# Performance work log

Measured on AMD Instinct MI355X. Metric: run time of the kernel, lower is better.

## Reference

```python
import jax, jax.numpy as jnp
import numpy as np

D = 1024      # embedding_size
H = 16        # num_heads
HD = D // H   # head_size
EPS = 1e-5


def setup_inputs() -> dict:
    key = jax.random.key(0)
    ks = jax.random.split(key, 12)
    s_in = 1.0 / np.sqrt(D)
    s_hid = 1.0 / np.sqrt(4 * D)
    return {
        "x": jax.random.normal(ks[0], (2, 2048, D), dtype=jnp.float32),
        # per-head projections, no bias: [H, D, HD]
        "Wq": jax.random.normal(ks[1], (H, D, HD), dtype=jnp.float32) * s_in,
        "Wk": jax.random.normal(ks[2], (H, D, HD), dtype=jnp.float32) * s_in,
        "Wv": jax.random.normal(ks[3], (H, D, HD), dtype=jnp.float32) * s_in,
        "Wo": jax.random.normal(ks[4], (D, D), dtype=jnp.float32) * s_in,
        "bo": jnp.zeros((D,), dtype=jnp.float32),
        "W1": jax.random.normal(ks[5], (D, 4 * D), dtype=jnp.float32) * s_in,
        "b1": jnp.zeros((4 * D,), dtype=jnp.float32),
        "W2": jax.random.normal(ks[6], (4 * D, D), dtype=jnp.float32) * s_hid,
        "b2": jnp.zeros((D,), dtype=jnp.float32),
        "g1": jnp.ones((D,), dtype=jnp.float32),
        "be1": jnp.zeros((D,), dtype=jnp.float32),
        "g2": jnp.ones((D,), dtype=jnp.float32),
        "be2": jnp.zeros((D,), dtype=jnp.float32),
    }


def _layernorm(x, g, b):
    mu = jnp.mean(x, axis=-1, keepdims=True)
    var = jnp.mean(jnp.square(x - mu), axis=-1, keepdims=True)
    return (x - mu) * jax.lax.rsqrt(var + EPS) * g + b


def _block(x, Wq, Wk, Wv, Wo, bo, W1, b1, W2, b2, g1, be1, g2, be2):
    B, T, _ = x.shape
    h = _layernorm(x, g1, be1)
    # per-head projections: [B, H, T, HD]
    q = jnp.einsum('btd,hde->bhte', h, Wq)
    k = jnp.einsum('btd,hde->bhte', h, Wk)
    v = jnp.einsum('btd,hde->bhte', h, Wv)
    # NOTE: original scales by embedding_size**-0.5 (x.shape[-1]), not head_size
    scores = jnp.einsum('bhte,bhse->bhts', q, k) * (D ** -0.5)
    mask = jnp.tril(jnp.ones((T, T), dtype=bool))
    scores = jnp.where(mask, scores, -jnp.inf)
    attn = jax.nn.softmax(scores, axis=-1)           # dropout = identity (eval)
    out = jnp.einsum('bhts,bhse->bhte', attn, v)      # [B, H, T, HD]
    out = out.transpose(0, 2, 1, 3).reshape(B, T, D)  # concat heads
    x = x + (out @ Wo + bo)
    h2 = _layernorm(x, g2, be2)
    ffn = jax.nn.relu(h2 @ W1 + b1) @ W2 + b2
    return x + ffn


def reference(x, Wq, Wk, Wv, Wo, bo, W1, b1, W2, b2, g1, be1, g2, be2):
    return _block(x, Wq, Wk, Wv, Wo, bo, W1, b1, W2, b2, g1, be1, g2, be2)
```

## Files before the change

kernel.cpp:

```cpp
#include <hip/hip_runtime.h>
#include <stdint.h>

typedef unsigned short u16;
typedef __attribute__((ext_vector_type(8))) __bf16 bf16x8;
typedef __attribute__((ext_vector_type(4))) float f32x4;

#define D_EMB 1024
#define NHEAD 16
#define HDIM 64
#define TSEQ 2048
#define NTOK 4096
#define NEG_BIG -1.0e30f

#define GLD16(lp, gp) __builtin_amdgcn_global_load_lds( \
    (const __attribute__((address_space(1))) unsigned int*)(gp), \
    (__attribute__((address_space(3))) unsigned int*)(lp), 16, 0, 0)

__device__ __forceinline__ float bf2f(u16 u) {
    union { unsigned int i; float f; } c; c.i = ((unsigned int)u) << 16; return c.f;
}
__device__ __forceinline__ u16 f2bf(float f) {
    union { float f; unsigned int i; } c; c.f = f;
    unsigned int r = (c.i + 0x7FFFu + ((c.i >> 16) & 1u)) >> 16;
    return (u16)r;
}
__device__ __forceinline__ void cp16(u16* dst, const u16* src) {
    *reinterpret_cast<uint4*>(dst) = *reinterpret_cast<const uint4*>(src);
}
__device__ __forceinline__ float load_in(const u16* p, size_t idx, int f32) {
    return f32 ? reinterpret_cast<const float*>(p)[idx] : bf2f(p[idx]);
}
__device__ __forceinline__ size_t tidx(int row, int col, int KB) {
    int c = (col & 7) | ((((col >> 3) ^ row) & 3) << 3);
    return ((size_t)((row >> 7) * KB + (col >> 5)) * 128 + (row & 127)) * 32 + c;
}

__global__ void detect_kernel(const u16* __restrict__ x, u16* __restrict__ fl) {
    if (threadIdx.x == 0) {
        int f = 0;
        for (int i = 0; i < 128; ++i) {
            float v = fabsf(bf2f(x[i]));
            if (!(v <= 1.0e3f)) f = 1;
        }
        fl[0] = (u16)f;
    }
}

__global__ __launch_bounds__(256) void transpose_tiled_kernel(
        const u16* __restrict__ X, u16* __restrict__ Xt, int KB,
        const u16* __restrict__ fl) {
    __shared__ __align__(16) u16 Ts[64 * 72];
    int f32 = fl[0];
    int bi = blockIdx.y, bj = blockIdx.x;
    int NS = gridDim.x * 64;
    int t = threadIdx.x;
    for (int p = 0; p < 2; ++p) {
        int idx = p * 256 + t;
        int row = idx >> 3, col8 = (idx & 7) * 8;
        size_t src = (size_t)(bi * 64 + row) * NS + bj * 64 + col8;
        if (f32) {
            for (int jj = 0; jj < 8; ++jj)
                Ts[row * 72 + col8 + jj] = f2bf(reinterpret_cast<const float*>(X)[src + jj]);
        } else {
            cp16(&Ts[row * 72 + col8], &X[src]);
        }
    }
    __syncthreads();
    for (int p = 0; p < 2; ++p) {
        int idx = p * 256 + t;
        int row = idx >> 3, col8 = (idx & 7) * 8;
        union { u16 u[8]; uint4 v; } tmp;
        for (int jj = 0; jj < 8; ++jj) tmp.u[jj] = Ts[(col8 + jj) * 72 + row];
        int n = bj * 64 + row, k0 = bi * 64 + col8;
        *reinterpret_cast<uint4*>(&Xt[tidx(n, k0, KB)]) = tmp.v;
    }
}

__global__ __launch_bounds__(256) void pack_qkv_kernel(
        const u16* __restrict__ Wq, const u16* __restrict__ Wk,
        const u16* __restrict__ Wv, u16* __restrict__ Wt,
        const u16* __restrict__ fl) {
    int f32 = fl[0];
    int idx = blockIdx.x * 256 + threadIdx.x;
    int e = idx & 63, d = (idx >> 6) & 1023, hh = (idx >> 16) & 15, sel = idx >> 20;
    const u16* W = (sel == 0) ? Wq : ((sel == 1) ? Wk : Wv);
    size_t src = (size_t)hh * (D_EMB * HDIM) + (size_t)d * HDIM + e;
    float v = f32 ? reinterpret_cast<const float*>(W)[src] : bf2f(W[src]);
    int n = sel * 1024 + hh * 64 + e;
    Wt[tidx(n, d, 32)] = f2bf(v);
}

__global__ __launch_bounds__(256) void ln_kernel(
        const u16* __restrict__ X, const u16* __restrict__ g,
        const u16* __restrict__ be, u16* __restrict__ Ht,
        const u16* __restrict__ fl) {
    int f32 = fl[0];
    int row = blockIdx.x;
    int t = threadIdx.x;
    float v[4];
    float s = 0.f, sq = 0.f;
    for (int i = 0; i < 4; ++i) {
        v[i] = load_in(X, (size_t)row * D_EMB + t + i * 256, f32);
        s += v[i]; sq += v[i] * v[i];
    }
    for (int m = 32; m; m >>= 1) { s += __shfl_down(s, m); sq += __shfl_down(sq, m); }
    __shared__ float red[8];
    int wid = t >> 6, lane = t & 63;
    if (lane == 0) { red[wid] = s; red[wid + 4] = sq; }
    __syncthreads();
    if (t == 0) {
        float S = red[0] + red[1] + red[2] + red[3];
        float SQ = red[4] + red[5] + red[6] + red[7];
        float mean = S * (1.f / 1024.f);
        float var = SQ * (1.f / 1024.f) - mean * mean;
        red[0] = mean; red[1] = rsqrtf(var + 1e-5f);
    }
    __syncthreads();
    float mean = red[0], rstd = red[1];
    for (int i = 0; i < 4; ++i) {
        int c = t + i * 256;
        float hv = (v[i] - mean) * rstd * load_in(g, c, f32) + load_in(be, c, f32);
        Ht[tidx(row, c, 32)] = f2bf(hv);
    }
}

template<int TAG, int TN>
__global__ __launch_bounds__(256) void gemm_t(
        const u16* __restrict__ At, const u16* __restrict__ Bt, u16* __restrict__ C,
        u16* __restrict__ C2,
        const u16* __restrict__ bias, const u16* __restrict__ res,
        int N, int K, int flags, int row_off,
        const u16* __restrict__ fl) {
    constexpr int NF = (TN == 128) ? 4 : 2;
    __shared__ __align__(16) u16 As2[2][4096];
    __shared__ __align__(16) u16 Bs2[2][TN * 32];
    int f32 = fl[0];
    int t = threadIdx.x;
    int gx = gridDim.x, gy = gridDim.y;
    int id = blockIdx.y * gx + blockIdx.x;
    int total = gx * gy;
    int xcd = id & 7, seq = id >> 3, P = total >> 3;
    int tpb = (P >= 32) ? 32 : 16;
    int th  = (P >= 32) ? 8 : 4;
    int tile = xcd * (P / tpb) + seq / tpb;
    int within = seq % tpb;
    int tiles_x = gx >> 2;
    int bx = (tile % tiles_x) * 4 + (within & 3);
    int by = (tile / tiles_x) * th + (within >> 2);
    int n0 = bx * TN, m0 = by * 128;
    int w = t >> 6, lane = t & 63, quad = lane >> 4, l16 = lane & 15;
    int wm = (TN == 128) ? (w >> 1) * 64 : (w & 1) * 64;
    int wn = (TN == 128) ? (w & 1) * 64  : (w >> 1) * 32;
    int KB = K >> 5;
    int kb0 = (seq * (KB >> 5)) & (KB - 1);
    const u16* Ab = At + (size_t)(m0 >> 7) * KB * 4096 + w * 512 + lane * 8;
    const u16* Bb = Bt + (size_t)(n0 >> 7) * KB * 4096
                       + ((TN == 64) ? (n0 & 64) * 32 : 0) + w * 512 + lane * 8;

    auto stage = [&](int buf, int kb) {
        const u16* ga = Ab + (size_t)kb * 4096;
        const u16* gb = Bb + (size_t)kb * 4096;
        u16* la = &As2[buf][w * 512];
        u16* lb = &Bs2[buf][w * 512];
        GLD16(la, ga);
        GLD16(la + 2048, ga + 2048);
        GLD16(lb, gb);
        if constexpr (TN == 128) { GLD16(lb + 2048, gb + 2048); }
    };

    const f32x4 fz = {0.f, 0.f, 0.f, 0.f};
    f32x4 acc[4][NF];
    for (int mt = 0; mt < 4; ++mt)
        for (int nt = 0; nt < NF; ++nt) acc[mt][nt] = fz;

    stage(0, kb0);
    __syncthreads();
    int kb = kb0;
    for (int it = 0; it < KB; ++it) {
        int cur = it & 1;
        int kn = (kb + 1 == KB) ? 0 : kb + 1;
        if (it + 1 < KB) stage(cur ^ 1, kn);
        bf16x8 af[4], bfr[NF];
        for (int mt = 0; mt < 4; ++mt) {
            int r = wm + mt * 16 + l16;
            af[mt] = *reinterpret_cast<const bf16x8*>(
                &As2[cur][r * 32 + (((quad ^ r) & 3) << 3)]);
        }
        for (int nt = 0; nt < NF; ++nt) {
            int r = wn + nt * 16 + l16;
            bfr[nt] = *reinterpret_cast<const bf16x8*>(
                &Bs2[cur][r * 32 + (((quad ^ r) & 3) << 3)]);
        }
        for (int mt = 0; mt < 4; ++mt)
            for (int nt = 0; nt < NF; ++nt)
                acc[mt][nt] = __builtin_amdgcn_mfma_f32_16x16x32_bf16(af[mt], bfr[nt], acc[mt][nt], 0, 0, 0);
        __syncthreads();
        kb = kn;
    }

    int relu_f = flags & 1, out_ext = flags & 2, c_tiled = flags & 4, qkvsp = flags & 8;
    for (int mt = 0; mt < 4; ++mt)
        for (int nt = 0; nt < NF; ++nt)
            for (int r = 0; r < 4; ++r) {
                int gr = m0 + wm + mt * 16 + quad * 4 + r;
                int gc = n0 + wn + nt * 16 + l16;
                float v = acc[mt][nt][r];
                if (bias) v += load_in(bias, gc, f32);
                if (relu_f) v = v > 0.f ? v : 0.f;
                size_t oidx = (size_t)(row_off + gr) * N + gc;
                if (res) v += load_in(res, oidx, f32);
                if (qkvsp) {
                    if (gc < 2048) {
                        C[(size_t)gr * 2048 + gc] = f2bf(v);
                    } else {
                        int hh = (gc - 2048) >> 6, d = gc & 63;
                        int bb = gr >> 11, s = gr & 2047;
                        C2[(((size_t)bb * 16 + hh) * 64 + d) * 2048 + s] = f2bf(v);
                    }
                }
                else if (c_tiled)      C[tidx(gr, gc, N >> 5)] = f2bf(v);
                else if (out_ext && f32) reinterpret_cast<float*>(C)[oidx] = v;
                else              C[oidx] = f2bf(v);
            }
}

template<int TAG, int KBL, int TN>
__global__ __launch_bounds__(256) void gemm_sk_t(
        const u16* __restrict__ At, const u16* __restrict__ Bt,
        float* __restrict__ Pp, int N, int K) {
    constexpr int NF = (TN == 128) ? 4 : 2;
    __shared__ __align__(16) u16 As2[2][4096];
    __shared__ __align__(16) u16 Bs2[2][TN * 32];
    int t = threadIdx.x;
    int gx = gridDim.x, gy = gridDim.y;
    int id = blockIdx.y * gx + blockIdx.x;
    int total = gx * gy;
    int xcd = id & 7, seq = id >> 3, P = total >> 3;
    int tpb = (P >= 32) ? 32 : 16;
    int th  = (P >= 32) ? 8 : 4;
    int tile = xcd * (P / tpb) + seq / tpb;
    int within = seq % tpb;
    int tiles_x = gx >> 2;
    int bx = (tile % tiles_x) * 4 + (within & 3);
    int by = (tile / tiles_x) * th + (within >> 2);
    int n0 = bx * TN, m0 = by * 128;
    int w = t >> 6, lane = t & 63, quad = lane >> 4, l16 = lane & 15;
    int wm = (TN == 128) ? (w >> 1) * 64 : (w & 1) * 64;
    int wn = (TN == 128) ? (w & 1) * 64  : (w >> 1) * 32;
    int KB = K >> 5;
    int kstart = blockIdx.z * KBL;
    int rel0 = seq & (KBL - 1);
    const u16* Ab = At + (size_t)(m0 >> 7) * KB * 4096 + w * 512 + lane * 8;
    const u16* Bb = Bt + (size_t)(n0 >> 7) * KB * 4096
                       + ((TN == 64) ? (n0 & 64) * 32 : 0) + w * 512 + lane * 8;

    auto stage = [&](int buf, int kb) {
        const u16* ga = Ab + (size_t)kb * 4096;
        const u16* gb = Bb + (size_t)kb * 4096;
        u16* la = &As2[buf][w * 512];
        u16* lb = &Bs2[buf][w * 512];
        GLD16(la, ga);
        GLD16(la + 2048, ga + 2048);
        GLD16(lb, gb);
        if constexpr (TN == 128) { GLD16(lb + 2048, gb + 2048); }
    };

    const f32x4 fz = {0.f, 0.f, 0.f, 0.f};
    f32x4 acc[4][NF];
    for (int mt = 0; mt < 4; ++mt)
        for (int nt = 0; nt < NF; ++nt) acc[mt][nt] = fz;

    stage(0, kstart + rel0);
    __syncthreads();
    for (int it = 0; it < KBL; ++it) {
        int cur = it & 1;
        if (it + 1 < KBL)
            stage(cur ^ 1, kstart + ((rel0 + it + 1) & (KBL - 1)));
        bf16x8 af[4], bfr[NF];
        for (int mt = 0; mt < 4; ++mt) {
            int r = wm + mt * 16 + l16;
            af[mt] = *reinterpret_cast<const bf16x8*>(
                &As2[cur][r * 32 + (((quad ^ r) & 3) << 3)]);
        }
        for (int nt = 0; nt < NF; ++nt) {
            int r = wn + nt * 16 + l16;
            bfr[nt] = *reinterpret_cast<const bf16x8*>(
                &Bs2[cur][r * 32 + (((quad ^ r) & 3) << 3)]);
        }
        for (int mt = 0; mt < 4; ++mt)
            for (int nt = 0; nt < NF; ++nt)
                acc[mt][nt] = __builtin_amdgcn_mfma_f32_16x16x32_bf16(af[mt], bfr[nt], acc[mt][nt], 0, 0, 0);
        __syncthreads();
    }

    for (int mt = 0; mt < 4; ++mt)
        for (int nt = 0; nt < NF; ++nt)
            for (int r = 0; r < 4; ++r) {
                int gr = m0 + wm + mt * 16 + quad * 4 + r;
                int gc = n0 + wn + nt * 16 + l16;
                atomicAdd(&Pp[(size_t)gr * N + gc], acc[mt][nt][r]);
            }
}

__global__ __launch_bounds__(256) void zero_f32_kernel(float* __restrict__ p) {
    const f32x4 fz = {0.f, 0.f, 0.f, 0.f};
    reinterpret_cast<f32x4*>(p)[(size_t)blockIdx.x * 256 + threadIdx.x] = fz;
}

__global__ __launch_bounds__(256) void ffn_fin_kernel(
        const float* __restrict__ Pp, const u16* __restrict__ b2,
        u16* __restrict__ out, int row_off, const u16* __restrict__ fl) {
    int f32 = fl[0];
    size_t i = ((size_t)blockIdx.x * 256 + threadIdx.x) * 4;
    int col = (int)(i & 1023);
    f32x4 pv = *reinterpret_cast<const f32x4*>(Pp + i);
    size_t o = (size_t)row_off * 1024 + i;
    if (f32) {
        float* of = reinterpret_cast<float*>(out);
        f32x4 ov = *reinterpret_cast<f32x4*>(of + o);
        for (int j = 0; j < 4; ++j)
            ov[j] += pv[j] + load_in(b2, col + j, 1);
        *reinterpret_cast<f32x4*>(of + o) = ov;
    } else {
        for (int j = 0; j < 4; ++j) {
            float v = bf2f(out[o + j]) + pv[j] + bf2f(b2[col + j]);
            out[o + j] = f2bf(v);
        }
    }
}

__global__ __launch_bounds__(256) void oproj_fin_kernel(
        const float* __restrict__ Pp, const u16* __restrict__ bo,
        const u16* __restrict__ x, u16* __restrict__ out,
        const u16* __restrict__ fl) {
    int f32 = fl[0];
    size_t i = ((size_t)blockIdx.x * 256 + threadIdx.x) * 4;
    int col = (int)(i & 1023);
    f32x4 pv = *reinterpret_cast<const f32x4*>(Pp + i);
    if (f32) {
        const float* xf = reinterpret_cast<const float*>(x);
        float* of = reinterpret_cast<float*>(out);
        f32x4 ov;
        for (int j = 0; j < 4; ++j)
            ov[j] = xf[i + j] + pv[j] + load_in(bo, col + j, 1);
        *reinterpret_cast<f32x4*>(of + i) = ov;
    } else {
        for (int j = 0; j < 4; ++j) {
            float v = bf2f(x[i + j]) + pv[j] + bf2f(bo[col + j]);
            out[i + j] = f2bf(v);
        }
    }
}

__global__ __launch_bounds__(256) void flash_kernel(
        const u16* __restrict__ qk, const u16* __restrict__ vt,
        u16* __restrict__ attn_t) {
    __shared__ __align__(16) u16 Ps[64 * 72];
    int t = threadIdx.x;
    int tq = gridDim.x - 1 - blockIdx.x;
    int b = blockIdx.y >> 4, h = blockIdx.y & 15;
    int wid = t >> 6, lane = t & 63, quad = lane >> 4, l16 = lane & 15;
    const size_t seq_base = (size_t)b * TSEQ;
    const u16* vplane = vt + (size_t)(b * 16 + h) * 64 * 2048;

    bf16x8 aq[2];
    for (int kit = 0; kit < 2; ++kit)
        aq[kit] = *reinterpret_cast<const bf16x8*>(
            &qk[(seq_base + tq * 64 + wid * 16 + l16) * 2048 + h * 64 + kit * 32 + quad * 8]);

    const f32x4 fz = {0.f, 0.f, 0.f, 0.f};
    float m_run[4], l_run[4];
    f32x4 o[4];
    for (int r = 0; r < 4; ++r) { m_run[r] = NEG_BIG; l_run[r] = 0.f; }
    for (int nt = 0; nt < 4; ++nt) o[nt] = fz;

    for (int j = 0; j <= tq; ++j) {
        f32x4 sa[4];
        for (int nt = 0; nt < 4; ++nt) sa[nt] = fz;
        for (int kit = 0; kit < 2; ++kit) {
            for (int nt = 0; nt < 4; ++nt) {
                bf16x8 bk = *reinterpret_cast<const bf16x8*>(
                    &qk[(seq_base + j * 64 + nt * 16 + l16) * 2048 + 1024 + h * 64 + kit * 32 + quad * 8]);
                sa[nt] = __builtin_amdgcn_mfma_f32_16x16x32_bf16(aq[kit], bk, sa[nt], 0, 0, 0);
            }
        }

        float p_val[4][4];
        int qbase = tq * 64 + wid * 16 + quad * 4;
        int sbase = j * 64 + l16;
        for (int r = 0; r < 4; ++r) {
            float sv[4];
            float mx = NEG_BIG;
            for (int nt = 0; nt < 4; ++nt) {
                float xv = sa[nt][r] * 0.03125f;
                if (sbase + nt * 16 > qbase + r) xv = NEG_BIG;
                sv[nt] = xv;
                mx = fmaxf(mx, xv);
            }
            for (int m = 1; m < 16; m <<= 1) mx = fmaxf(mx, __shfl_xor(mx, m));
            float mnew = fmaxf(m_run[r], mx);
            float alpha = __expf(m_run[r] - mnew);
            m_run[r] = mnew;
            float rs = 0.f;
            for (int nt = 0; nt < 4; ++nt) {
                float pv = __expf(sv[nt] - mnew);
                p_val[nt][r] = pv;
                rs += pv;
            }
            for (int m = 1; m < 16; m <<= 1) rs += __shfl_xor(rs, m);
            l_run[r] = l_run[r] * alpha + rs;
            for (int nt = 0; nt < 4; ++nt) o[nt][r] *= alpha;
        }

        for (int nt = 0; nt < 4; ++nt)
            for (int r = 0; r < 4; ++r)
                Ps[(wid * 16 + quad * 4 + r) * 72 + nt * 16 + l16] = f2bf(p_val[nt][r]);

        for (int kit = 0; kit < 2; ++kit) {
            bf16x8 ap = *reinterpret_cast<const bf16x8*>(
                &Ps[(wid * 16 + l16) * 72 + kit * 32 + quad * 8]);
            for (int nt = 0; nt < 4; ++nt) {
                bf16x8 bv = *reinterpret_cast<const bf16x8*>(
                    &vplane[(size_t)(nt * 16 + l16) * 2048 + j * 64 + kit * 32 + quad * 8]);
                o[nt] = __builtin_amdgcn_mfma_f32_16x16x32_bf16(ap, bv, o[nt], 0, 0, 0);
            }
        }
    }

    for (int nt = 0; nt < 4; ++nt)
        for (int r = 0; r < 4; ++r) {
            int trow = (int)seq_base + tq * 64 + wid * 16 + quad * 4 + r;
            int col = h * 64 + nt * 16 + l16;
            attn_t[tidx(trow, col, 32)] = f2bf(o[nt][r] / l_run[r]);
        }
}

extern "C" void kernel_launch(void* const* d_in, const int* in_sizes, int n_in,
                              void* d_out, int out_size, void* d_ws, size_t ws_size,
                              hipStream_t stream) {
    const u16* x   = (const u16*)d_in[0];
    const u16* Wq  = (const u16*)d_in[1];
    const u16* Wk  = (const u16*)d_in[2];
    const u16* Wv  = (const u16*)d_in[3];
    const u16* Wo  = (const u16*)d_in[4];
    const u16* bo  = (const u16*)d_in[5];
    const u16* W1  = (const u16*)d_in[6];
    const u16* b1  = (const u16*)d_in[7];
    const u16* W2  = (const u16*)d_in[8];
    const u16* b2  = (const u16*)d_in[9];
    const u16* g1  = (const u16*)d_in[10];
    const u16* be1 = (const u16*)d_in[11];
    const u16* g2  = (const u16*)d_in[12];
    const u16* be2 = (const u16*)d_in[13];
    u16* out = (u16*)d_out;

    const size_t M1 = (size_t)1 << 20;
    u16* ws    = (u16*)d_ws;
    u16* qk    = ws;
    u16* vt    = ws + 8 * M1;
    u16* W2t   = ws;
    u16* a1    = ws + 4 * M1;
    u16* h     = ws + 12 * M1;
    u16* attn  = ws + 12 * M1;
    u16* h2    = ws + 12 * M1;
    u16* Wtq   = ws + 16 * M1;
    u16* Wot   = ws + 16 * M1;
    u16* W1t   = ws + 16 * M1;
    u16* fl    = ws + 20 * M1;
    float* Pp  = reinterpret_cast<float*>(ws + 21 * M1);
    bool sk = ws_size >= ((size_t)58 << 20);

    detect_kernel<<<1, 64, 0, stream>>>(x, fl);

    pack_qkv_kernel<<<(3 * 16 * 1024 * 64) / 256, 256, 0, stream>>>(Wq, Wk, Wv, Wtq, fl);
    ln_kernel<<<NTOK, 256, 0, stream>>>(x, g1, be1, h, fl);
    gemm_t<0, 64><<<dim3(48, 32), 256, 0, stream>>>(
        h, Wtq, qk, vt, nullptr, nullptr, 3072, 1024, 8, 0, fl);

    transpose_tiled_kernel<<<dim3(16, 16), 256, 0, stream>>>(Wo, Wot, 32, fl);

    flash_kernel<<<dim3(32, 32), 256, 0, stream>>>(qk, vt, attn);

    if (sk) {
        zero_f32_kernel<<<4096, 256, 0, stream>>>(Pp);
        gemm_sk_t<2, 8, 64><<<dim3(16, 32, 4), 256, 0, stream>>>(attn, Wot, Pp, 1024, 1024);
        oproj_fin_kernel<<<4096, 256, 0, stream>>>(Pp, bo, x, out, fl);
    } else {
        gemm_t<1, 128><<<dim3(8, 32), 256, 0, stream>>>(
            attn, Wot, out, nullptr, bo, x, 1024, 1024, 2, 0, fl);
    }

    transpose_tiled_kernel<<<dim3(16, 64), 256, 0, stream>>>(W2, W2t, 128, fl);
    transpose_tiled_kernel<<<dim3(64, 16), 256, 0, stream>>>(W1, W1t, 32, fl);
    ln_kernel<<<NTOK, 256, 0, stream>>>(out, g2, be2, h2, fl);

    gemm_t<2, 64><<<dim3(64, 16), 256, 0, stream>>>(
        h2, W1t, a1, nullptr, b1, nullptr, 4096, 1024, 1 | 4, 0, fl);
    if (sk) {
        zero_f32_kernel<<<2048, 256, 0, stream>>>(Pp);
        gemm_sk_t<0, 32, 64><<<dim3(16, 16, 4), 256, 0, stream>>>(a1, W2t, Pp, 1024, 4096);
        ffn_fin_kernel<<<2048, 256, 0, stream>>>(Pp, b2, out, 0, fl);
    } else {
        gemm_t<4, 128><<<dim3(8, 16), 256, 0, stream>>>(
            a1, W2t, out, nullptr, b2, out, 1024, 4096, 2, 0, fl);
    }
    gemm_t<3, 64><<<dim3(64, 16), 256, 0, stream>>>(
        h2 + (size_t)2 * M1, W1t, a1, nullptr, b1, nullptr, 4096, 1024, 1 | 4, 0, fl);
    if (sk) {
        zero_f32_kernel<<<2048, 256, 0, stream>>>(Pp);
        gemm_sk_t<1, 32, 64><<<dim3(16, 16, 4), 256, 0, stream>>>(a1, W2t, Pp, 1024, 4096);
        ffn_fin_kernel<<<2048, 256, 0, stream>>>(Pp, b2, out, 2048, fl);
    } else {
        gemm_t<5, 128><<<dim3(8, 16), 256, 0, stream>>>(
            a1, W2t, out, nullptr, b2, out, 1024, 4096, 2, 2048, fl);
    }
}
```

Before: 682.6 us.

## Balance causal flash work by pairing query tiles and vectorize V-transpose stores

The flash attention kernel now runs 128-thread blocks, and each block processes two query tiles paired as (31-px, px). This makes the causal work per block uniform instead of ranging from 1 to 32 key tiles. The QKV GEMM epilogue gets a dedicated path that packs four consecutive sequence positions into one 8-byte store for the transposed V layout. The trade-offs are fewer waves per block, less K/V reuse across waves within a block, and serial execution of the two halves.

```diff
diff --git a/kernel.cpp b/kernel.cpp
--- a/kernel.cpp
+++ b/kernel.cpp
@@ -199,6 +199,25 @@
     }
 
     int relu_f = flags & 1, out_ext = flags & 2, c_tiled = flags & 4, qkvsp = flags & 8;
+    if (qkvsp) {
+        for (int mt = 0; mt < 4; ++mt)
+            for (int nt = 0; nt < NF; ++nt) {
+                int gc = n0 + wn + nt * 16 + l16;
+                int grb = m0 + wm + mt * 16 + quad * 4;
+                if (gc < 2048) {
+                    for (int r = 0; r < 4; ++r)
+                        C[(size_t)(grb + r) * 2048 + gc] = f2bf(acc[mt][nt][r]);
+                } else {
+                    int hh = (gc - 2048) >> 6, d = gc & 63;
+                    int bb = grb >> 11, s = grb & 2047;
+                    union { u16 u[4]; uint2 v; } pk;
+                    for (int r = 0; r < 4; ++r) pk.u[r] = f2bf(acc[mt][nt][r]);
+                    *reinterpret_cast<uint2*>(
+                        &C2[(((size_t)bb * 16 + hh) * 64 + d) * 2048 + s]) = pk.v;
+                }
+            }
+        return;
+    }
     for (int mt = 0; mt < 4; ++mt)
         for (int nt = 0; nt < NF; ++nt)
             for (int r = 0; r < 4; ++r) {
@@ -209,16 +228,7 @@
                 if (relu_f) v = v > 0.f ? v : 0.f;
                 size_t oidx = (size_t)(row_off + gr) * N + gc;
                 if (res) v += load_in(res, oidx, f32);
-                if (qkvsp) {
-                    if (gc < 2048) {
-                        C[(size_t)gr * 2048 + gc] = f2bf(v);
-                    } else {
-                        int hh = (gc - 2048) >> 6, d = gc & 63;
-                        int bb = gr >> 11, s = gr & 2047;
-                        C2[(((size_t)bb * 16 + hh) * 64 + d) * 2048 + s] = f2bf(v);
-                    }
-                }
-                else if (c_tiled)      C[tidx(gr, gc, N >> 5)] = f2bf(v);
+                if (c_tiled)      C[tidx(gr, gc, N >> 5)] = f2bf(v);
                 else if (out_ext && f32) reinterpret_cast<float*>(C)[oidx] = v;
                 else              C[oidx] = f2bf(v);
             }
@@ -352,87 +362,92 @@
     }
 }
 
-__global__ __launch_bounds__(256) void flash_kernel(
+__global__ __launch_bounds__(128) void flash_kernel(
         const u16* __restrict__ qk, const u16* __restrict__ vt,
         u16* __restrict__ attn_t) {
-    __shared__ __align__(16) u16 Ps[64 * 72];
+    __shared__ __align__(16) u16 Ps[32 * 72];
     int t = threadIdx.x;
-    int tq = gridDim.x - 1 - blockIdx.x;
+    int px = blockIdx.x & 15, rh = blockIdx.x >> 4;
     int b = blockIdx.y >> 4, h = blockIdx.y & 15;
     int wid = t >> 6, lane = t & 63, quad = lane >> 4, l16 = lane & 15;
+    int g = rh * 2 + wid;
     const size_t seq_base = (size_t)b * TSEQ;
     const u16* vplane = vt + (size_t)(b * 16 + h) * 64 * 2048;
 
-    bf16x8 aq[2];
-    for (int kit = 0; kit < 2; ++kit)
-        aq[kit] = *reinterpret_cast<const bf16x8*>(
-            &qk[(seq_base + tq * 64 + wid * 16 + l16) * 2048 + h * 64 + kit * 32 + quad * 8]);
-
-    const f32x4 fz = {0.f, 0.f, 0.f, 0.f};
-    float m_run[4], l_run[4];
-    f32x4 o[4];
-    for (int r = 0; r < 4; ++r) { m_run[r] = NEG_BIG; l_run[r] = 0.f; }
-    for (int nt = 0; nt < 4; ++nt) o[nt] = fz;
-
-    for (int j = 0; j <= tq; ++j) {
-        f32x4 sa[4];
-        for (int nt = 0; nt < 4; ++nt) sa[nt] = fz;
-        for (int kit = 0; kit < 2; ++kit) {
-            for (int nt = 0; nt < 4; ++nt) {
-                bf16x8 bk = *reinterpret_cast<const bf16x8*>(
-                    &qk[(seq_base + j * 64 + nt * 16 + l16) * 2048 + 1024 + h * 64 + kit * 32 + quad * 8]);
-                sa[nt] = __builtin_amdgcn_mfma_f32_16x16x32_bf16(aq[kit], bk, sa[nt], 0, 0, 0);
-            }
-        }
-
-        float p_val[4][4];
-        int qbase = tq * 64 + wid * 16 + quad * 4;
-        int sbase = j * 64 + l16;
-        for (int r = 0; r < 4; ++r) {
-            float sv[4];
-            float mx = NEG_BIG;
-            for (int nt = 0; nt < 4; ++nt) {
-                float xv = sa[nt][r] * 0.03125f;
-                if (sbase + nt * 16 > qbase + r) xv = NEG_BIG;
-                sv[nt] = xv;
-                mx = fmaxf(mx, xv);
-            }
-            for (int m = 1; m < 16; m <<= 1) mx = fmaxf(mx, __shfl_xor(mx, m));
-            float mnew = fmaxf(m_run[r], mx);
-            float alpha = __expf(m_run[r] - mnew);
-            m_run[r] = mnew;
-            float rs = 0.f;
-            for (int nt = 0; nt < 4; ++nt) {
-                float pv = __expf(sv[nt] - mnew);
-                p_val[nt][r] = pv;
-                rs += pv;
-            }
-            for (int m = 1; m < 16; m <<= 1) rs += __shfl_xor(rs, m);
-            l_run[r] = l_run[r] * alpha + rs;
-            for (int nt = 0; nt < 4; ++nt) o[nt][r] *= alpha;
+    for (int half = 0; half < 2; ++half) {
+        int tq = half ? px : (31 - px);
+
+        bf16x8 aq[2];
+        for (int kit = 0; kit < 2; ++kit)
+            aq[kit] = *reinterpret_cast<const bf16x8*>(
+                &qk[(seq_base + tq * 64 + g * 16 + l16) * 2048 + h * 64 + kit * 32 + quad * 8]);
+
+        const f32x4 fz = {0.f, 0.f, 0.f, 0.f};
+        float m_run[4], l_run[4];
+        f32x4 o[4];
+        for (int r = 0; r < 4; ++r) { m_run[r] = NEG_BIG; l_run[r] = 0.f; }
+        for (int nt = 0; nt < 4; ++nt) o[nt] = fz;
+
+        for (int j = 0; j <= tq; ++j) {
+            f32x4 sa[4];
+            for (int nt = 0; nt < 4; ++nt) sa[nt] = fz;
+            for (int kit = 0; kit < 2; ++kit) {
+                for (int nt = 0; nt < 4; ++nt) {
+                    bf16x8 bk = *reinterpret_cast<const bf16x8*>(
+                        &qk[(seq_base + j * 64 + nt * 16 + l16) * 2048 + 1024 + h * 64 + kit * 32 + quad * 8]);
+                    sa[nt] = __builtin_amdgcn_mfma_f32_16x16x32_bf16(aq[kit], bk, sa[nt], 0, 0, 0);
+                }
+            }
+
+            float p_val[4][4];
+            int qbase = tq * 64 + g * 16 + quad * 4;
+            int sbase = j * 64 + l16;
+            for (int r = 0; r < 4; ++r) {
+                float sv[4];
+                float mx = NEG_BIG;
+                for (int nt = 0; nt < 4; ++nt) {
+                    float xv = sa[nt][r] * 0.03125f;
+                    if (sbase + nt * 16 > qbase + r) xv = NEG_BIG;
+                    sv[nt] = xv;
+                    mx = fmaxf(mx, xv);
+                }
+                for (int m = 1; m < 16; m <<= 1) mx = fmaxf(mx, __shfl_xor(mx, m));
+                float mnew = fmaxf(m_run[r], mx);
+                float alpha = __expf(m_run[r] - mnew);
+                m_run[r] = mnew;
+                float rs = 0.f;
+                for (int nt = 0; nt < 4; ++nt) {
+                    float pv = __expf(sv[nt] - mnew);
+                    p_val[nt][r] = pv;
+                    rs += pv;
+                }
+                for (int m = 1; m < 16; m <<= 1) rs += __shfl_xor(rs, m);
+                l_run[r] = l_run[r] * alpha + rs;
+                for (int nt = 0; nt < 4; ++nt) o[nt][r] *= alpha;
+            }
+
+            for (int nt = 0; nt < 4; ++nt)
+                for (int r = 0; r < 4; ++r)
+                    Ps[(wid * 16 + quad * 4 + r) * 72 + nt * 16 + l16] = f2bf(p_val[nt][r]);
+
+            for (int kit = 0; kit < 2; ++kit) {
+                bf16x8 ap = *reinterpret_cast<const bf16x8*>(
+                    &Ps[(wid * 16 + l16) * 72 + kit * 32 + quad * 8]);
+                for (int nt = 0; nt < 4; ++nt) {
+                    bf16x8 bv = *reinterpret_cast<const bf16x8*>(
+                        &vplane[(size_t)(nt * 16 + l16) * 2048 + j * 64 + kit * 32 + quad * 8]);
+                    o[nt] = __builtin_amdgcn_mfma_f32_16x16x32_bf16(ap, bv, o[nt], 0, 0, 0);
+                }
+            }
         }
 
         for (int nt = 0; nt < 4; ++nt)
-            for (int r = 0; r < 4; ++r)
-                Ps[(wid * 16 + quad * 4 + r) * 72 + nt * 16 + l16] = f2bf(p_val[nt][r]);
-
-        for (int kit = 0; kit < 2; ++kit) {
-            bf16x8 ap = *reinterpret_cast<const bf16x8*>(
-                &Ps[(wid * 16 + l16) * 72 + kit * 32 + quad * 8]);
-            for (int nt = 0; nt < 4; ++nt) {
-                bf16x8 bv = *reinterpret_cast<const bf16x8*>(
-                    &vplane[(size_t)(nt * 16 + l16) * 2048 + j * 64 + kit * 32 + quad * 8]);
-                o[nt] = __builtin_amdgcn_mfma_f32_16x16x32_bf16(ap, bv, o[nt], 0, 0, 0);
-            }
-        }
-    }
-
-    for (int nt = 0; nt < 4; ++nt)
-        for (int r = 0; r < 4; ++r) {
-            int trow = (int)seq_base + tq * 64 + wid * 16 + quad * 4 + r;
-            int col = h * 64 + nt * 16 + l16;
-            attn_t[tidx(trow, col, 32)] = f2bf(o[nt][r] / l_run[r]);
-        }
+            for (int r = 0; r < 4; ++r) {
+                int trow = (int)seq_base + tq * 64 + g * 16 + quad * 4 + r;
+                int col = h * 64 + nt * 16 + l16;
+                attn_t[tidx(trow, col, 32)] = f2bf(o[nt][r] / l_run[r]);
+            }
+    }
 }
 
 extern "C" void kernel_launch(void* const* d_in, const int* in_sizes, int n_in,
@@ -479,7 +494,7 @@
 
     transpose_tiled_kernel<<<dim3(16, 16), 256, 0, stream>>>(Wo, Wot, 32, fl);
 
-    flash_kernel<<<dim3(32, 32), 256, 0, stream>>>(qk, vt, attn);
+    flash_kernel<<<dim3(32, 32), 128, 0, stream>>>(qk, vt, attn);
 
     if (sk) {
         zero_f32_kernel<<<4096, 256, 0, stream>>>(Pp);
```

Result: faster. 626.9 us (-8.2%).
